# Optimization experiments

Measured on AMD Instinct MI355X. Metric: run time of the kernel, lower is better.

The kernel has to match this reference:

```python
import jax, jax.numpy as jnp
import numpy as np

N, M, K = 100000, 50000, 8   # num vertices, num hyperedges, fixed hyperedge size
DIN, DOUT = 128, 128

def setup_inputs() -> dict:
    key = jax.random.key(0)
    k1, k2, k3 = jax.random.split(key, 3)
    X = jax.random.normal(k1, (N, DIN), jnp.float32)
    vertex = jax.random.randint(k2, (M * K,), 0, N)          # member vertices, flattened
    edges = jnp.repeat(jnp.arange(M), K)                     # hyperedge id per entry (sorted)
    W = jax.random.normal(k3, (DIN, DOUT), jnp.float32) / np.sqrt(DIN)
    b = jnp.zeros((DOUT,), jnp.float32)
    return {"X": X, "vertex": vertex, "edges": edges, "W": W, "b": b}

def reference(X, vertex, edges, W, b):
    # theta: Linear(in, out) applied BEFORE graph construction (as in dhg.HyperGCNConv)
    Y = X @ W + b                              # [N, DOUT]
    verts = vertex.reshape(M, K)               # hyperedge membership (edges = repeat(arange(M), K))
    feats = Y[verts]                           # [M, K, DOUT] gather
    # pairwise squared distances within each hyperedge
    sq = jnp.sum(feats * feats, axis=-1)                      # [M, K]
    d2 = sq[:, :, None] + sq[:, None, :] - 2.0 * jnp.einsum('mkd,mld->mkl', feats, feats)
    flat = jnp.argmax(d2.reshape(M, K * K), axis=1)
    ui, vi = flat // K, flat % K                              # argmax-distance pair positions
    u = jnp.take_along_axis(verts, ui[:, None], 1)[:, 0]      # [M]
    v = jnp.take_along_axis(verts, vi[:, None], 1)[:, 0]      # [M]
    w = jnp.float32(1.0 / (2 * K - 3))                        # HyperGCN mediator weight
    pos = jnp.arange(K)
    med = ((pos[None, :] != ui[:, None]) & (pos[None, :] != vi[:, None])).astype(Y.dtype)  # [M,K]
    # graph edges: (u,v) + (u,m),(v,m) for each mediator m; masked entries get weight 0
    src = jnp.concatenate([u, jnp.repeat(u, K), jnp.repeat(v, K)])
    dst = jnp.concatenate([v, verts.reshape(-1), verts.reshape(-1)])
    wts = jnp.concatenate([jnp.full((M,), w, Y.dtype), (med * w).reshape(-1), (med * w).reshape(-1)])
    # GCN smoothing: D^{-1/2} (A + I) D^{-1/2} Y with symmetric A, duplicate edges summed
    deg = jnp.ones((N,), Y.dtype).at[src].add(wts).at[dst].add(wts)
    dinv = jax.lax.rsqrt(deg)
    Xs = Y * dinv[:, None]
    out = Xs                                                  # self-loop term
    out = out.at[dst].add(wts[:, None] * Xs[src])
    out = out.at[src].add(wts[:, None] * Xs[dst])
    out = out * dinv[:, None]
    return jax.nn.relu(out)                                   # is_last=False -> ReLU (dropout=0)
```

## Files before the change

kernel.cpp:

```cpp
#include <hip/hip_runtime.h>
#include <hip/hip_bf16.h>

#define NV 100000
#define ME 50000
#define NINC (ME * 8)
#define NBLK ((NV + 255) / 256)
#define NRBG ((NV + 127) / 128)
constexpr float WMED = 1.0f / 13.0f;

typedef __attribute__((ext_vector_type(8))) short bf16x8;
typedef __attribute__((ext_vector_type(4))) float f32x4;

static __device__ inline void cvt_split8(const float4& a, const float4& b,
                                         bf16x8& hi, bf16x8& lo) {
    const float v[8] = {a.x, a.y, a.z, a.w, b.x, b.y, b.z, b.w};
    #pragma unroll
    for (int j = 0; j < 8; ++j) {
        __hip_bfloat16 h = __float2bfloat16(v[j]);
        const float hf = __bfloat162float(h);
        __hip_bfloat16 l = __float2bfloat16(v[j] - hf);
        union { __hip_bfloat16 b; short s; } uh{h}, ul{l};
        hi[j] = uh.s;
        lo[j] = ul.s;
    }
}

__global__ __launch_bounds__(256) void k_wsplit(const float* __restrict__ W,
                                                short* __restrict__ Wg) {
    const int idx = blockIdx.x * 256 + threadIdx.x;
    const int k = idx >> 7;
    const int c = idx & 127;
    const float w = W[idx];
    __hip_bfloat16 h = __float2bfloat16(w);
    const float hf = __bfloat162float(h);
    __hip_bfloat16 l = __float2bfloat16(w - hf);
    const int cb = c >> 6, gp = (c >> 4) & 3, m = c & 15;
    const int s = k >> 5, qq = (k >> 3) & 3, j = k & 7;
    const int base = cb * 1024 + (s * 4 + gp) * 64 + qq * 16 + m;
    union { __hip_bfloat16 b; short s; } uh{h}, ul{l};
    Wg[(long)base * 8 + j] = uh.s;
    Wg[(long)(2048 + base) * 8 + j] = ul.s;
}

__global__ __launch_bounds__(256, 4) void k_gemm(const float* __restrict__ X,
                                                 const uint4* __restrict__ Wg,
                                                 const float* __restrict__ bias,
                                                 float* __restrict__ Y,
                                                 __hip_bfloat16* __restrict__ Ybf) {
    const int t = threadIdx.x;
    const int wv = t >> 6;
    const int L  = t & 63;
    const int m  = L & 15;
    const int q  = L >> 4;

    const int rb = blockIdx.x >> 1;
    const int cb = blockIdx.x & 1;

    const int row_base = rb * 128 + wv * 32;
    int r0 = row_base + m;      if (r0 > NV - 1) r0 = NV - 1;
    int r1 = row_base + 16 + m; if (r1 > NV - 1) r1 = NV - 1;
    const float* p0 = X + (long)r0 * 128 + q * 8;
    const float* p1 = X + (long)r1 * 128 + q * 8;

    const bf16x8* Whf = (const bf16x8*)Wg + cb * 1024;
    const bf16x8* Wlf = (const bf16x8*)Wg + 2048 + cb * 1024;

    f32x4 acc[2][4];
    #pragma unroll
    for (int tt = 0; tt < 2; ++tt)
        #pragma unroll
        for (int g = 0; g < 4; ++g)
            acc[tt][g] = (f32x4){0.f, 0.f, 0.f, 0.f};

    float4 Ac0 = *(const float4*)(p0);
    float4 Ac1 = *(const float4*)(p0 + 4);
    float4 Ac2 = *(const float4*)(p1);
    float4 Ac3 = *(const float4*)(p1 + 4);

    #pragma unroll
    for (int s = 0; s < 4; ++s) {
        float4 An0, An1, An2, An3;
        if (s < 3) {
            An0 = *(const float4*)(p0 + (s + 1) * 32);
            An1 = *(const float4*)(p0 + (s + 1) * 32 + 4);
            An2 = *(const float4*)(p1 + (s + 1) * 32);
            An3 = *(const float4*)(p1 + (s + 1) * 32 + 4);
        }
        bf16x8 ah0, al0, ah1, al1;
        cvt_split8(Ac0, Ac1, ah0, al0);
        cvt_split8(Ac2, Ac3, ah1, al1);
        #pragma unroll
        for (int g = 0; g < 4; ++g) {
            const bf16x8 bh = Whf[(s * 4 + g) * 64 + L];
            const bf16x8 bl = Wlf[(s * 4 + g) * 64 + L];
            acc[0][g] = __builtin_amdgcn_mfma_f32_16x16x32_bf16(ah0, bh, acc[0][g], 0, 0, 0);
            acc[0][g] = __builtin_amdgcn_mfma_f32_16x16x32_bf16(ah0, bl, acc[0][g], 0, 0, 0);
            acc[0][g] = __builtin_amdgcn_mfma_f32_16x16x32_bf16(al0, bh, acc[0][g], 0, 0, 0);
            acc[1][g] = __builtin_amdgcn_mfma_f32_16x16x32_bf16(ah1, bh, acc[1][g], 0, 0, 0);
            acc[1][g] = __builtin_amdgcn_mfma_f32_16x16x32_bf16(ah1, bl, acc[1][g], 0, 0, 0);
            acc[1][g] = __builtin_amdgcn_mfma_f32_16x16x32_bf16(al1, bh, acc[1][g], 0, 0, 0);
        }
        if (s < 3) { Ac0 = An0; Ac1 = An1; Ac2 = An2; Ac3 = An3; }
    }

    float bc[4];
    #pragma unroll
    for (int g = 0; g < 4; ++g) bc[g] = bias[cb * 64 + g * 16 + m];

    #pragma unroll
    for (int tt = 0; tt < 2; ++tt) {
        #pragma unroll
        for (int r = 0; r < 4; ++r) {
            const int row = row_base + tt * 16 + q * 4 + r;
            float vg[4], vn[4];
            #pragma unroll
            for (int g = 0; g < 4; ++g) {
                vg[g] = acc[tt][g][r] + bc[g];
                vn[g] = __shfl_xor(vg[g], 1);
            }
            if (row < NV) {
                #pragma unroll
                for (int g = 0; g < 4; ++g)
                    Y[(long)row * 128 + cb * 64 + g * 16 + m] = vg[g];
                if ((L & 1) == 0) {
                    #pragma unroll
                    for (int g = 0; g < 4; ++g) {
                        __hip_bfloat162 h2;
                        h2.x = __float2bfloat16(vg[g]);
                        h2.y = __float2bfloat16(vn[g]);
                        *(__hip_bfloat162*)(Ybf + (long)row * 128 + cb * 64 + g * 16 + m) = h2;
                    }
                }
            }
        }
    }
}

__global__ __launch_bounds__(256) void k_edge(const float* __restrict__ Y,
                                              const int* __restrict__ vertex,
                                              int* __restrict__ uvpos) {
    __shared__ float sF[4][8 * 132 + 8];
    const int wid = threadIdx.x >> 6;
    const int lane = threadIdx.x & 63;
    const int m = blockIdx.x * 4 + wid;
    float* F = sF[wid];
    float* T8 = F + 8 * 132;

    const int c = lane & 31;
    const int half = lane >> 5;

    float part[4];
    #pragma unroll
    for (int i = 0; i < 4; ++i) {
        const int row = 2 * i + half;
        const int vr = vertex[m * 8 + row];
        const float4 v = *(const float4*)(Y + (long)vr * 128 + c * 4);
        *(float4*)(F + row * 132 + c * 4) = v;
        const float s = v.x * v.x + v.y * v.y + v.z * v.z + v.w * v.w;
        part[i] = (c >= 16) ? s : 0.0f;
    }
    #pragma unroll
    for (int off = 1; off <= 8; off <<= 1) {
        #pragma unroll
        for (int i = 0; i < 4; ++i) part[i] += __shfl_xor(part[i], off);
    }
    if (c == 16) {
        #pragma unroll
        for (int i = 0; i < 4; ++i) T8[2 * i + half] = part[i];
    }

    const int k = lane >> 3, l = lane & 7;

    const int h = (k > l) ? 64 : 0;
    float acc = 0.0f;
    const float4* ra = (const float4*)(F + k * 132 + h);
    const float4* rbp = (const float4*)(F + l * 132 + h);
    #pragma unroll
    for (int d4 = 0; d4 < 16; ++d4) {
        const float4 a = ra[d4], b = rbp[d4];
        acc = fmaf(a.x, b.x, acc);
        acc = fmaf(a.y, b.y, acc);
        acc = fmaf(a.z, b.z, acc);
        acc = fmaf(a.w, b.w, acc);
    }

    const float accT = __shfl(acc, l * 8 + k);
    const float s1k = __shfl(acc, k * 9);
    const float s1l = __shfl(acc, l * 9);
    const float Tk = T8[k];
    const float Tl = T8[l];
    float v = (k == l) ? 0.0f
                       : ((s1k + Tk) + (s1l + Tl) - 2.0f * (acc + accT));

    int idx = lane;
    #pragma unroll
    for (int off = 32; off >= 1; off >>= 1) {
        const float ov = __shfl_xor(v, off);
        const int oi = __shfl_xor(idx, off);
        if (ov > v || (ov == v && oi < idx)) { v = ov; idx = oi; }
    }
    if (lane == 0) uvpos[m] = idx;
}

__global__ __launch_bounds__(256) void k_init(int* __restrict__ cnt,
                                              int* __restrict__ rowptr) {
    const int i = blockIdx.x * 256 + threadIdx.x;
    if (i < NV) cnt[i] = 0;
    if (i == 0) rowptr[NV] = NINC;
}

__global__ __launch_bounds__(256) void k_hist(const int* __restrict__ vertex,
                                              int* __restrict__ cnt) {
    const int j = blockIdx.x * 256 + threadIdx.x;
    if (j < NINC) atomicAdd(cnt + vertex[j], 1);
}

__global__ __launch_bounds__(256) void k_scan1(const int* __restrict__ cnt,
                                               int* __restrict__ bsum) {
    __shared__ int s[256];
    const int t = threadIdx.x;
    const int i = blockIdx.x * 256 + t;
    s[t] = (i < NV) ? cnt[i] : 0;
    __syncthreads();
    #pragma unroll
    for (int off = 128; off >= 1; off >>= 1) {
        if (t < off) s[t] += s[t + off];
        __syncthreads();
    }
    if (t == 0) bsum[blockIdx.x] = s[0];
}

__global__ __launch_bounds__(64) void k_scan2(const int* __restrict__ bsum,
                                              int* __restrict__ boff) {
    const int lane = threadIdx.x;
    int running = 0;
    for (int c = 0; c * 64 < NBLK; ++c) {
        const int idx = c * 64 + lane;
        int v = (idx < NBLK) ? bsum[idx] : 0;
        int x = v;
        #pragma unroll
        for (int off = 1; off < 64; off <<= 1) {
            const int n = __shfl_up(x, off);
            if (lane >= off) x += n;
        }
        if (idx < NBLK) boff[idx] = running + x - v;
        running += __shfl(x, 63);
    }
}

__global__ __launch_bounds__(256) void k_scan3(const int* __restrict__ cnt,
                                               const int* __restrict__ boff,
                                               int* __restrict__ rowptr,
                                               int* __restrict__ fill) {
    __shared__ int s[256];
    const int t = threadIdx.x;
    const int i = blockIdx.x * 256 + t;
    const int v = (i < NV) ? cnt[i] : 0;
    s[t] = v;
    __syncthreads();
    #pragma unroll
    for (int off = 1; off < 256; off <<= 1) {
        const int add = (t >= off) ? s[t - off] : 0;
        __syncthreads();
        s[t] += add;
        __syncthreads();
    }
    if (i < NV) {
        const int excl = boff[blockIdx.x] + s[t] - v;
        rowptr[i] = excl;
        fill[i] = excl;
    }
}

__global__ __launch_bounds__(256) void k_fill(const int* __restrict__ vertex,
                                              const int* __restrict__ uvpos,
                                              int* __restrict__ fill,
                                              int* __restrict__ entries) {
    const int j = blockIdx.x * 256 + threadIdx.x;
    if (j < NINC) {
        const int v = vertex[j];
        const int m = j >> 3, p = j & 7;
        const int idx = uvpos[m];
        const int role = (p == (idx >> 3) || p == (idx & 7)) ? 0 : 1;
        const int slot = atomicAdd(fill + v, 1);
        entries[slot] = (m << 1) | role;
    }
}

__global__ __launch_bounds__(256) void k_deg(const int* __restrict__ rowptr,
                                             const int* __restrict__ entries,
                                             float* __restrict__ deg) {
    const int i = blockIdx.x * 256 + threadIdx.x;
    if (i >= NV) return;
    const int start = rowptr[i], end = rowptr[i + 1];
    float d = 1.0f;
    for (int e = start; e < end; ++e)
        d += (entries[e] & 1) ? (2.0f * WMED) : (7.0f * WMED);
    deg[i] = d;
}

__global__ __launch_bounds__(256) void k_sp(const __hip_bfloat16* __restrict__ Ybf,
                                            const int* __restrict__ vertex,
                                            const int* __restrict__ uvpos,
                                            const float* __restrict__ deg,
                                            __hip_bfloat162* __restrict__ SP) {
    const int wid = threadIdx.x >> 6;
    const int lane = threadIdx.x & 63;
    const int m = blockIdx.x * 4 + wid;

    const int idx = uvpos[m];
    const int ui = idx >> 3, vi = idx & 7;

    float S0 = 0.f, S1 = 0.f, U0 = 0.f, U1 = 0.f, V0 = 0.f, V1 = 0.f;
    #pragma unroll
    for (int p = 0; p < 8; ++p) {
        const int vp = vertex[m * 8 + p];
        const float di = rsqrtf(deg[vp]);
        const __hip_bfloat162 y2 =
            ((const __hip_bfloat162*)(Ybf + (long)vp * 128))[lane];
        const float r0 = __bfloat162float(y2.x) * di;
        const float r1 = __bfloat162float(y2.y) * di;
        S0 += r0; S1 += r1;
        if (p == ui) { U0 = r0; U1 = r1; }
        if (p == vi) { V0 = r0; V1 = r1; }
    }
    __hip_bfloat162 s2, p2;
    s2.x = __float2bfloat16(WMED * S0);
    s2.y = __float2bfloat16(WMED * S1);
    p2.x = __float2bfloat16(WMED * (U0 + V0));
    p2.y = __float2bfloat16(WMED * (U1 + V1));
    SP[(long)(2 * m) * 64 + lane] = s2;
    SP[(long)(2 * m + 1) * 64 + lane] = p2;
}

__global__ __launch_bounds__(256) void k_gather(const float* __restrict__ Y,
                                                const float* __restrict__ deg,
                                                const int* __restrict__ rowptr,
                                                const int* __restrict__ entries,
                                                const __hip_bfloat162* __restrict__ SP,
                                                float* __restrict__ out) {
    const int wid = threadIdx.x >> 6;
    const int lane = threadIdx.x & 63;
    const int i = blockIdx.x * 4 + wid;

    const int start = rowptr[i], end = rowptr[i + 1];
    const int degc = end - start;
    const int tl = (lane < degc) ? entries[start + lane] : 0;

    const float din = rsqrtf(deg[i]);
    const float2 y = *(const float2*)(Y + (long)i * 128 + lane * 2);
    const float xs0 = y.x * din;
    const float xs1 = y.y * din;

    float a0 = 0.f, a1 = 0.f;
    float fnuv = 0.f;
    const int dmain = (degc < 64) ? degc : 64;

    for (int e = 0; e < dmain; e += 4) {
        const int j1 = (e + 1 < dmain) ? e + 1 : e;
        const int j2 = (e + 2 < dmain) ? e + 2 : e;
        const int j3 = (e + 3 < dmain) ? e + 3 : e;
        const float m1 = (e + 1 < dmain) ? 1.f : 0.f;
        const float m2 = (e + 2 < dmain) ? 1.f : 0.f;
        const float m3 = (e + 3 < dmain) ? 1.f : 0.f;
        const int t0 = __shfl(tl, e);
        const int t1 = __shfl(tl, j1);
        const int t2 = __shfl(tl, j2);
        const int t3 = __shfl(tl, j3);
        const __hip_bfloat162 T0 = SP[(long)t0 * 64 + lane];
        const __hip_bfloat162 T1 = SP[(long)t1 * 64 + lane];
        const __hip_bfloat162 T2 = SP[(long)t2 * 64 + lane];
        const __hip_bfloat162 T3 = SP[(long)t3 * 64 + lane];
        fnuv += (float)((t0 & 1) ^ 1) + m1 * (float)((t1 & 1) ^ 1)
              + m2 * (float)((t2 & 1) ^ 1) + m3 * (float)((t3 & 1) ^ 1);
        a0 += __bfloat162float(T0.x) + m1 * __bfloat162float(T1.x)
            + m2 * __bfloat162float(T2.x) + m3 * __bfloat162float(T3.x);
        a1 += __bfloat162float(T0.y) + m1 * __bfloat162float(T1.y)
            + m2 * __bfloat162float(T2.y) + m3 * __bfloat162float(T3.y);
    }
    for (int e2 = start + 64; e2 < end; ++e2) {
        const int t = entries[e2];
        const __hip_bfloat162 T = SP[(long)t * 64 + lane];
        fnuv += (float)((t & 1) ^ 1);
        a0 += __bfloat162float(T.x);
        a1 += __bfloat162float(T.y);
    }

    const float self = 1.0f - WMED * fnuv;
    a0 = fmaf(self, xs0, a0);
    a1 = fmaf(self, xs1, a1);
    float2 o;
    o.x = fmaxf(a0 * din, 0.0f);
    o.y = fmaxf(a1 * din, 0.0f);
    *(float2*)(out + (long)i * 128 + lane * 2) = o;
}

extern "C" void kernel_launch(void* const* d_in, const int* in_sizes, int n_in,
                              void* d_out, int out_size, void* d_ws, size_t ws_size,
                              hipStream_t stream) {
    const float* X      = (const float*)d_in[0];
    const int*   vertex = (const int*)d_in[1];
    const float* W      = (const float*)d_in[3];
    const float* bias   = (const float*)d_in[4];
    float* out = (float*)d_out;

    float* Y              = (float*)d_ws;
    __hip_bfloat16* Ybf   = (__hip_bfloat16*)(Y + (long)NV * 128);
    __hip_bfloat162* SP   = (__hip_bfloat162*)(Ybf + (long)NV * 128);
    float* deg            = (float*)((__hip_bfloat16*)SP + (long)2 * ME * 128);
    int*   uvpos          = (int*)(deg + NV);
    int*   cnt            = uvpos + ME;
    int*   rowptr         = cnt + NV;
    int*   fill           = rowptr + NV + 1;
    int*   bsum           = fill + NV;
    int*   boff           = bsum + NBLK;
    int*   entries        = boff + NBLK;
    char*  pW             = (char*)(entries + NINC);
    uint4* Wg             = (uint4*)(((uintptr_t)pW + 15) & ~(uintptr_t)15);

    k_wsplit<<<64, 256, 0, stream>>>(W, (short*)Wg);
    k_gemm <<<NRBG * 2, 256, 0, stream>>>(X, Wg, bias, Y, Ybf);
    k_edge <<<ME / 4, 256, 0, stream>>>(Y, vertex, uvpos);
    k_init <<<NBLK, 256, 0, stream>>>(cnt, rowptr);
    k_hist <<<(NINC + 255) / 256, 256, 0, stream>>>(vertex, cnt);
    k_scan1<<<NBLK, 256, 0, stream>>>(cnt, bsum);
    k_scan2<<<1, 64, 0, stream>>>(bsum, boff);
    k_scan3<<<NBLK, 256, 0, stream>>>(cnt, boff, rowptr, fill);
    k_fill <<<(NINC + 255) / 256, 256, 0, stream>>>(vertex, uvpos, fill, entries);
    k_deg  <<<NBLK, 256, 0, stream>>>(rowptr, entries, deg);
    k_sp   <<<ME / 4, 256, 0, stream>>>(Ybf, vertex, uvpos, deg, SP);
    k_gather<<<NV / 4, 256, 0, stream>>>(Y, deg, rowptr, entries, SP, out);
}
```

Baseline: 276.8 us.

## Compute hyperedge Gram matrix with bf16 split MFMA instead of LDS FMA loops

```diff
diff --git a/kernel.cpp b/kernel.cpp
--- a/kernel.cpp
+++ b/kernel.cpp
@@ -139,58 +139,46 @@
 __global__ __launch_bounds__(256) void k_edge(const float* __restrict__ Y,
                                               const int* __restrict__ vertex,
                                               int* __restrict__ uvpos) {
-    __shared__ float sF[4][8 * 132 + 8];
     const int wid = threadIdx.x >> 6;
     const int lane = threadIdx.x & 63;
     const int m = blockIdx.x * 4 + wid;
-    float* F = sF[wid];
-    float* T8 = F + 8 * 132;
-
-    const int c = lane & 31;
-    const int half = lane >> 5;
-
-    float part[4];
-    #pragma unroll
-    for (int i = 0; i < 4; ++i) {
-        const int row = 2 * i + half;
-        const int vr = vertex[m * 8 + row];
-        const float4 v = *(const float4*)(Y + (long)vr * 128 + c * 4);
-        *(float4*)(F + row * 132 + c * 4) = v;
-        const float s = v.x * v.x + v.y * v.y + v.z * v.z + v.w * v.w;
-        part[i] = (c >= 16) ? s : 0.0f;
-    }
-    #pragma unroll
-    for (int off = 1; off <= 8; off <<= 1) {
-        #pragma unroll
-        for (int i = 0; i < 4; ++i) part[i] += __shfl_xor(part[i], off);
-    }
-    if (c == 16) {
-        #pragma unroll
-        for (int i = 0; i < 4; ++i) T8[2 * i + half] = part[i];
+
+    const int x = lane & 15;
+    const int q = lane >> 4;
+    const int vr = vertex[m * 8 + (x & 7)];
+    const float* rp = Y + (long)vr * 128 + q * 8;
+
+    float4 A0[4], A1[4];
+    #pragma unroll
+    for (int s = 0; s < 4; ++s) {
+        A0[s] = *(const float4*)(rp + s * 32);
+        A1[s] = *(const float4*)(rp + s * 32 + 4);
+    }
+
+    f32x4 acc = (f32x4){0.f, 0.f, 0.f, 0.f};
+    #pragma unroll
+    for (int s = 0; s < 4; ++s) {
+        bf16x8 ah, al;
+        cvt_split8(A0[s], A1[s], ah, al);
+        acc = __builtin_amdgcn_mfma_f32_16x16x32_bf16(ah, ah, acc, 0, 0, 0);
+        acc = __builtin_amdgcn_mfma_f32_16x16x32_bf16(ah, al, acc, 0, 0, 0);
+        acc = __builtin_amdgcn_mfma_f32_16x16x32_bf16(al, ah, acc, 0, 0, 0);
     }
 
     const int k = lane >> 3, l = lane & 7;
-
-    const int h = (k > l) ? 64 : 0;
-    float acc = 0.0f;
-    const float4* ra = (const float4*)(F + k * 132 + h);
-    const float4* rbp = (const float4*)(F + l * 132 + h);
-    #pragma unroll
-    for (int d4 = 0; d4 < 16; ++d4) {
-        const float4 a = ra[d4], b = rbp[d4];
-        acc = fmaf(a.x, b.x, acc);
-        acc = fmaf(a.y, b.y, acc);
-        acc = fmaf(a.z, b.z, acc);
-        acc = fmaf(a.w, b.w, acc);
-    }
-
-    const float accT = __shfl(acc, l * 8 + k);
-    const float s1k = __shfl(acc, k * 9);
-    const float s1l = __shfl(acc, l * 9);
-    const float Tk = T8[k];
-    const float Tl = T8[l];
-    float v = (k == l) ? 0.0f
-                       : ((s1k + Tk) + (s1l + Tl) - 2.0f * (acc + accT));
+    const int srcG = l + 16 * (k >> 2);
+    const int srcK = k + 16 * (k >> 2);
+    const int srcL = l + 16 * (l >> 2);
+    float g = 0.f, sk = 0.f, sl = 0.f;
+    #pragma unroll
+    for (int r = 0; r < 4; ++r) {
+        const float tg = __shfl(acc[r], srcG);
+        const float tk = __shfl(acc[r], srcK);
+        const float tl = __shfl(acc[r], srcL);
+        if ((k & 3) == r) { g = tg; sk = tk; }
+        if ((l & 3) == r) sl = tl;
+    }
+    float v = sk + sl - 2.0f * g;
 
     int idx = lane;
     #pragma unroll
```

New measurement: 284.4 us. 1.03x slower.
